# Kernel optimization log

Measured on AMD Instinct MI355X. Metric: run time of the kernel, lower is better.

Reference implementation:

```python
import jax, jax.numpy as jnp
import numpy as np

NUM_HEADS = 16
MASK_VAL = -1e6  # d2l masked_softmax fill value


def setup_inputs() -> dict:
    key = jax.random.key(0)
    ks = jax.random.split(key, 8)
    B, S, D = 4, 1024, 1024
    scale = 1.0 / np.sqrt(D)
    inp = {
        "queries": jax.random.normal(ks[0], (B, S, D), dtype=jnp.float32),
        "keys": jax.random.normal(ks[1], (B, S, D), dtype=jnp.float32),
        "values": jax.random.normal(ks[2], (B, S, D), dtype=jnp.float32),
        "valid_lens": jax.random.randint(ks[3], (B,), 1, S + 1, dtype=jnp.int32),
        "W_q": jax.random.normal(ks[4], (D, D), dtype=jnp.float32) * scale,
        "W_k": jax.random.normal(ks[5], (D, D), dtype=jnp.float32) * scale,
        "W_v": jax.random.normal(ks[6], (D, D), dtype=jnp.float32) * scale,
        "W_o": jax.random.normal(ks[7], (D, D), dtype=jnp.float32) * scale,
    }
    return inp


def _split_heads(x, H):
    # [B, S, D] -> [B, H, S, d]
    B, S, D = x.shape
    return x.reshape(B, S, H, D // H).transpose(0, 2, 1, 3)


def reference(queries, keys, values, valid_lens, W_q, W_k, W_v, W_o):
    H = NUM_HEADS
    B, Sq, D = queries.shape
    Sk = keys.shape[1]
    d = D // H

    q = _split_heads(queries @ W_q.T, H)  # [B, H, Sq, d]
    k = _split_heads(keys @ W_k.T, H)     # [B, H, Sk, d]
    v = _split_heads(values @ W_v.T, H)   # [B, H, Sk, d]

    scores = jnp.einsum("bhqd,bhkd->bhqk", q, k) / jnp.sqrt(jnp.float32(d))
    # masked_softmax: mask key positions >= valid_len (per batch row)
    mask = jnp.arange(Sk)[None, None, None, :] < valid_lens[:, None, None, None]
    scores = jnp.where(mask, scores, MASK_VAL)
    attn = jax.nn.softmax(scores, axis=-1)  # dropout=0.0 -> identity

    out = jnp.einsum("bhqk,bhkd->bhqd", attn, v)  # [B, H, Sq, d]
    out = out.transpose(0, 2, 1, 3).reshape(B, Sq, D)
    return out @ W_o.T
```

## Files before the change

kernel.cpp:

```cpp
#include <hip/hip_runtime.h>

typedef unsigned short ushort_t;
typedef unsigned int uint32;
typedef __attribute__((ext_vector_type(8))) short short8;
typedef __attribute__((ext_vector_type(4))) float float4v;
typedef __attribute__((ext_vector_type(4))) unsigned short ushort4v;

#define NEG_INF (-__builtin_inff())

__device__ __forceinline__ ushort_t f2bf(float f) {
  uint32 u = __float_as_uint(f);
  u += 0x7fffu + ((u >> 16) & 1u);
  return (ushort_t)(u >> 16);
}

__device__ __forceinline__ void glds16(const void* g, void* l) {
  __builtin_amdgcn_global_load_lds(
      (__attribute__((address_space(1))) const void*)g,
      (__attribute__((address_space(3))) void*)l, 16, 0, 0);
}

struct CvtW {
  const float* in[4];
  ushort_t* out[4];
};

__global__ __launch_bounds__(256) void cvt_w_kernel(CvtW a) {
  const float* in = a.in[blockIdx.y];
  ushort_t* out = a.out[blockIdx.y];
  int i = blockIdx.x * 256 + threadIdx.x;
  float4v v = ((const float4v*)in)[i];
  ushort4v o;
  o.x = f2bf(v.x);
  o.y = f2bf(v.y);
  o.z = f2bf(v.z);
  o.w = f2bf(v.w);
  ((ushort4v*)out)[i] = o;
}

struct ProjArgs {
  const float* A[3];
  const ushort_t* B[3];
  ushort_t* C[3];
};

__global__ __launch_bounds__(256) void gemm_proj(ProjArgs pa, int M, int N,
                                                 int K) {
  __shared__ __align__(16) ushort_t Al[128][32];
  __shared__ __align__(16) ushort_t Bl[128][32];
  const int orig = blockIdx.x + (blockIdx.y << 3) + (blockIdx.z << 8);
  const int swz = (orig & 7) * 96 + (orig >> 3);
  const int bn = (swz & 7) * 128;
  const int bm = ((swz >> 3) & 31) * 128;
  const int z = swz >> 8;
  const float* A = pa.A[z];
  const ushort_t* B = pa.B[z];
  ushort_t* C = pa.C[z];
  const int tid = threadIdx.x;
  const int w = tid >> 6, lane = tid & 63;
  const int l15 = lane & 15, lhi = lane >> 4;

  const int wm = (w >> 1) * 64, wn = (w & 1) * 64;

  float4v zero4 = {0.f, 0.f, 0.f, 0.f};
  float4v acc[4][4];
  for (int i = 0; i < 4; i++)
    for (int j = 0; j < 4; j++) acc[i][j] = zero4;

  const int sr = tid >> 2;
  const int sc = tid & 3;
  const int ssw = sc ^ ((sr >> 1) & 3);
  const ushort_t* gb = B + (size_t)(bn + sr) * K + ssw * 8;
  char* lB = (char*)&Bl[0][0];
  const int wb = w * 1024;
  const float* gaf = A + (size_t)(bm + sr) * K + sc * 8;

  const int rsw8 = (lhi ^ ((l15 >> 1) & 3)) * 8;

  for (int kt = 0; kt < K; kt += 32) {
    glds16(gb + kt, lB + wb);
    glds16(gb + (size_t)64 * K + kt, lB + 4096 + wb);
#pragma unroll
    for (int rep = 0; rep < 2; rep++) {
      const int row = rep * 64 + sr;
      const float* p = gaf + (size_t)rep * 64 * K + kt;
      float4v u0 = ((const float4v*)p)[0];
      float4v u1 = ((const float4v*)p)[1];
      short8 sv;
      sv[0] = (short)f2bf(u0.x);
      sv[1] = (short)f2bf(u0.y);
      sv[2] = (short)f2bf(u0.z);
      sv[3] = (short)f2bf(u0.w);
      sv[4] = (short)f2bf(u1.x);
      sv[5] = (short)f2bf(u1.y);
      sv[6] = (short)f2bf(u1.z);
      sv[7] = (short)f2bf(u1.w);
      *(short8*)&Al[row][ssw * 8] = sv;
    }
    __syncthreads();
    short8 af[4], bfr[4];
#pragma unroll
    for (int mi = 0; mi < 4; mi++)
      af[mi] = *(const short8*)&Al[wm + mi * 16 + l15][rsw8];
#pragma unroll
    for (int ni = 0; ni < 4; ni++)
      bfr[ni] = *(const short8*)&Bl[wn + ni * 16 + l15][rsw8];
#pragma unroll
    for (int mi = 0; mi < 4; mi++)
#pragma unroll
      for (int ni = 0; ni < 4; ni++)
        acc[mi][ni] = __builtin_amdgcn_mfma_f32_16x16x32_bf16(
            af[mi], bfr[ni], acc[mi][ni], 0, 0, 0);
    __syncthreads();
  }

#pragma unroll
  for (int mi = 0; mi < 4; mi++)
#pragma unroll
    for (int ni = 0; ni < 4; ni++)
#pragma unroll
      for (int i = 0; i < 4; i++) {
        int row = bm + wm + mi * 16 + lhi * 4 + i;
        int col = bn + wn + ni * 16 + l15;
        C[(size_t)row * N + col] = f2bf(acc[mi][ni][i]);
      }
}

__global__ __launch_bounds__(256) void gemm_out(const ushort_t* __restrict__ A,
                                                const ushort_t* __restrict__ B,
                                                float* __restrict__ Cout, int M,
                                                int N, int K) {
  __shared__ __align__(16) ushort_t Al[128][32];
  __shared__ __align__(16) ushort_t Bl[128][32];
  const int orig = blockIdx.x + (blockIdx.y << 3);
  const int swz = (orig & 7) * 32 + (orig >> 3);
  const int bn = (swz & 7) * 128;
  const int bm = (swz >> 3) * 128;
  const int tid = threadIdx.x;
  const int w = tid >> 6, lane = tid & 63;
  const int l15 = lane & 15, lhi = lane >> 4;
  const int wm = (w >> 1) * 64, wn = (w & 1) * 64;

  float4v zero4 = {0.f, 0.f, 0.f, 0.f};
  float4v acc[4][4];
  for (int i = 0; i < 4; i++)
    for (int j = 0; j < 4; j++) acc[i][j] = zero4;

  const int sr = tid >> 2;
  const int sc = tid & 3;
  const int ssw = sc ^ ((sr >> 1) & 3);
  const ushort_t* ga = A + (size_t)(bm + sr) * K + ssw * 8;
  const ushort_t* gb = B + (size_t)(bn + sr) * K + ssw * 8;
  char* lA = (char*)&Al[0][0];
  char* lB = (char*)&Bl[0][0];
  const int wb = w * 1024;
  const int rsw8 = (lhi ^ ((l15 >> 1) & 3)) * 8;

  for (int kt = 0; kt < K; kt += 32) {
    glds16(ga + kt, lA + wb);
    glds16(ga + (size_t)64 * K + kt, lA + 4096 + wb);
    glds16(gb + kt, lB + wb);
    glds16(gb + (size_t)64 * K + kt, lB + 4096 + wb);
    __syncthreads();
    short8 af[4], bfr[4];
#pragma unroll
    for (int mi = 0; mi < 4; mi++)
      af[mi] = *(const short8*)&Al[wm + mi * 16 + l15][rsw8];
#pragma unroll
    for (int ni = 0; ni < 4; ni++)
      bfr[ni] = *(const short8*)&Bl[wn + ni * 16 + l15][rsw8];
#pragma unroll
    for (int mi = 0; mi < 4; mi++)
#pragma unroll
      for (int ni = 0; ni < 4; ni++)
        acc[mi][ni] = __builtin_amdgcn_mfma_f32_16x16x32_bf16(
            af[mi], bfr[ni], acc[mi][ni], 0, 0, 0);
    __syncthreads();
  }

#pragma unroll
  for (int mi = 0; mi < 4; mi++)
#pragma unroll
    for (int ni = 0; ni < 4; ni++)
#pragma unroll
      for (int i = 0; i < 4; i++) {
        int row = bm + wm + mi * 16 + lhi * 4 + i;
        int col = bn + wn + ni * 16 + l15;
        Cout[(size_t)row * N + col] = acc[mi][ni][i];
      }
}

__global__ __launch_bounds__(256) void transpose_v_kernel(
    const ushort_t* __restrict__ Vp, ushort_t* __restrict__ Vt) {
  __shared__ ushort_t tile[64][65];
  const int bx = blockIdx.x;
  const int b = bx >> 8, h = (bx >> 4) & 15, c = bx & 15;
  const int t = threadIdx.x;
#pragma unroll
  for (int i = 0; i < 16; i++) {
    int id = i * 256 + t;
    int tok = id >> 6, dd = id & 63;
    tile[tok][dd] = Vp[(size_t)(b * 1024 + c * 64 + tok) * 1024 + h * 64 + dd];
  }
  __syncthreads();
#pragma unroll
  for (int i = 0; i < 16; i++) {
    int id = i * 256 + t;
    int dd = id >> 6, tok = id & 63;
    Vt[(size_t)((b * 16 + h) * 64 + dd) * 1024 + c * 64 + tok] = tile[tok][dd];
  }
}

__global__ __launch_bounds__(64) void attn_kernel(
    const ushort_t* __restrict__ Qp, const ushort_t* __restrict__ Kp,
    const ushort_t* __restrict__ Vt, const int* __restrict__ valid_lens,
    ushort_t* __restrict__ Ob) {
  __shared__ __align__(16) ushort_t Plds[16][72];
  const int lane = threadIdx.x & 63;
  const int l15 = lane & 15, lhi = lane >> 4;
  const int bx = blockIdx.x;
  const int b = bx >> 10;
  const int h = (bx >> 6) & 15;
  const int qt = bx & 63;
  const int qrow0 = qt * 16;
  const int vlen = valid_lens[b];

  short8 qf0, qf1;
  {
    const ushort_t* qp =
        Qp + (size_t)(b * 1024 + qrow0 + l15) * 1024 + h * 64 + lhi * 8;
    qf0 = *(const short8*)qp;
    qf1 = *(const short8*)(qp + 32);
  }
  float4v zero4 = {0.f, 0.f, 0.f, 0.f};
  float4v o[4] = {zero4, zero4, zero4, zero4};
  float m_i[4] = {NEG_INF, NEG_INF, NEG_INF, NEG_INF};
  float l_i[4] = {0.f, 0.f, 0.f, 0.f};

  const ushort_t* kh = Kp + (size_t)b * 1024 * 1024 + h * 64;
  const ushort_t* vh = Vt + (size_t)(b * 16 + h) * 64 * 1024;

  for (int kt = 0; kt < 16; kt++) {
    const int k0 = kt * 64;
    if (k0 >= vlen) break;

    float4v s[4];
#pragma unroll
    for (int n = 0; n < 4; n++) {
      const ushort_t* kp = kh + (size_t)(k0 + n * 16 + l15) * 1024 + lhi * 8;
      short8 kf0 = *(const short8*)kp;
      short8 kf1 = *(const short8*)(kp + 32);
      s[n] = __builtin_amdgcn_mfma_f32_16x16x32_bf16(qf0, kf0, zero4, 0, 0, 0);
      s[n] = __builtin_amdgcn_mfma_f32_16x16x32_bf16(qf1, kf1, s[n], 0, 0, 0);
    }
    float pm[4] = {NEG_INF, NEG_INF, NEG_INF, NEG_INF};
#pragma unroll
    for (int n = 0; n < 4; n++) {
      const bool ok = (k0 + n * 16 + l15) < vlen;
#pragma unroll
      for (int i = 0; i < 4; i++) {
        float v = s[n][i] * 0.125f;
        v = ok ? v : -1e6f;
        s[n][i] = v;
        pm[i] = fmaxf(pm[i], v);
      }
    }
#pragma unroll
    for (int d = 1; d < 16; d <<= 1)
#pragma unroll
      for (int i = 0; i < 4; i++) pm[i] = fmaxf(pm[i], __shfl_xor(pm[i], d, 64));

    float alpha[4], rs[4];
#pragma unroll
    for (int i = 0; i < 4; i++) {
      float mn = fmaxf(m_i[i], pm[i]);
      alpha[i] = __expf(m_i[i] - mn);
      m_i[i] = mn;
      rs[i] = 0.f;
    }
#pragma unroll
    for (int n = 0; n < 4; n++)
#pragma unroll
      for (int i = 0; i < 4; i++) {
        float p = __expf(s[n][i] - m_i[i]);
        s[n][i] = p;
        rs[i] += p;
      }
#pragma unroll
    for (int d = 1; d < 16; d <<= 1)
#pragma unroll
      for (int i = 0; i < 4; i++) rs[i] += __shfl_xor(rs[i], d, 64);
#pragma unroll
    for (int i = 0; i < 4; i++) l_i[i] = l_i[i] * alpha[i] + rs[i];
#pragma unroll
    for (int n = 0; n < 4; n++)
#pragma unroll
      for (int i = 0; i < 4; i++) o[n][i] *= alpha[i];

#pragma unroll
    for (int n = 0; n < 4; n++)
#pragma unroll
      for (int i = 0; i < 4; i++)
        Plds[lhi * 4 + i][n * 16 + l15] = f2bf(s[n][i]);

#pragma unroll
    for (int c = 0; c < 2; c++) {
      short8 pa = *(const short8*)&Plds[l15][c * 32 + lhi * 8];
      const ushort_t* vb = vh + k0 + c * 32 + lhi * 8;
#pragma unroll
      for (int n = 0; n < 4; n++) {
        short8 vf = *(const short8*)(vb + (size_t)(n * 16 + l15) * 1024);
        o[n] = __builtin_amdgcn_mfma_f32_16x16x32_bf16(pa, vf, o[n], 0, 0, 0);
      }
    }
  }

#pragma unroll
  for (int n = 0; n < 4; n++)
#pragma unroll
    for (int i = 0; i < 4; i++) {
      float vout = o[n][i] / l_i[i];
      Ob[(size_t)(b * 1024 + qrow0 + lhi * 4 + i) * 1024 + h * 64 + n * 16 +
         l15] = f2bf(vout);
    }
}

extern "C" void kernel_launch(void* const* d_in, const int* in_sizes, int n_in,
                              void* d_out, int out_size, void* d_ws,
                              size_t ws_size, hipStream_t stream) {
  (void)in_sizes;
  (void)n_in;
  (void)out_size;
  (void)ws_size;
  const float* q = (const float*)d_in[0];
  const float* k = (const float*)d_in[1];
  const float* v = (const float*)d_in[2];
  const int* vl = (const int*)d_in[3];
  const float* Wq = (const float*)d_in[4];
  const float* Wk = (const float*)d_in[5];
  const float* Wv = (const float*)d_in[6];
  const float* Wo = (const float*)d_in[7];
  float* out = (float*)d_out;
  char* ws = (char*)d_ws;
  const size_t MB = 1u << 20;

  ushort_t* wqb = (ushort_t*)(ws + 0 * MB);
  ushort_t* wkb = (ushort_t*)(ws + 2 * MB);
  ushort_t* wvb = (ushort_t*)(ws + 4 * MB);
  ushort_t* wob = (ushort_t*)(ws + 6 * MB);
  ushort_t* Qp = (ushort_t*)(ws + 8 * MB);
  ushort_t* Kp = (ushort_t*)(ws + 16 * MB);
  ushort_t* Vp = (ushort_t*)(ws + 24 * MB);
  ushort_t* Vtp = (ushort_t*)(ws + 32 * MB);
  ushort_t* Ob = Vp;

  CvtW cw;
  cw.in[0] = Wq;
  cw.in[1] = Wk;
  cw.in[2] = Wv;
  cw.in[3] = Wo;
  cw.out[0] = wqb;
  cw.out[1] = wkb;
  cw.out[2] = wvb;
  cw.out[3] = wob;
  cvt_w_kernel<<<dim3(1024, 4), 256, 0, stream>>>(cw);

  ProjArgs pa;
  pa.A[0] = q;
  pa.A[1] = k;
  pa.A[2] = v;
  pa.B[0] = wqb;
  pa.B[1] = wkb;
  pa.B[2] = wvb;
  pa.C[0] = Qp;
  pa.C[1] = Kp;
  pa.C[2] = Vp;
  gemm_proj<<<dim3(8, 32, 3), 256, 0, stream>>>(pa, 4096, 1024, 1024);

  transpose_v_kernel<<<1024, 256, 0, stream>>>(Vp, Vtp);
  attn_kernel<<<4096, 64, 0, stream>>>(Qp, Kp, Vtp, vl, Ob);
  gemm_out<<<dim3(8, 32), 256, 0, stream>>>(Ob, wob, out, 4096, 1024, 1024);
}
```

Before: 233.8 us.

## Double-buffer LDS tiles in projection and output GEMMs to overlap loads

Both GEMM kernels now keep two LDS stages and prefetch the next K-tile while MFMAs run on the current one. The projection GEMM holds the fp32 A loads in registers and converts and stores them to LDS after the MFMAs. This halves the number of barriers per K step and hides global load latency, at the cost of double the LDS use and more registers. That may lower occupancy. The global_load_lds writes into the other buffer are issued before the compute, so correctness relies on the barrier at the end of each step.

```diff
diff --git a/kernel.cpp b/kernel.cpp
--- a/kernel.cpp
+++ b/kernel.cpp
@@ -46,8 +46,8 @@
 
 __global__ __launch_bounds__(256) void gemm_proj(ProjArgs pa, int M, int N,
                                                  int K) {
-  __shared__ __align__(16) ushort_t Al[128][32];
-  __shared__ __align__(16) ushort_t Bl[128][32];
+  __shared__ __align__(16) ushort_t Al[2][128][32];
+  __shared__ __align__(16) ushort_t Bl[2][128][32];
   const int orig = blockIdx.x + (blockIdx.y << 3) + (blockIdx.z << 8);
   const int swz = (orig & 7) * 96 + (orig >> 3);
   const int bn = (swz & 7) * 128;
@@ -59,7 +59,6 @@
   const int tid = threadIdx.x;
   const int w = tid >> 6, lane = tid & 63;
   const int l15 = lane & 15, lhi = lane >> 4;
-
   const int wm = (w >> 1) * 64, wn = (w & 1) * 64;
 
   float4v zero4 = {0.f, 0.f, 0.f, 0.f};
@@ -71,47 +70,78 @@
   const int sc = tid & 3;
   const int ssw = sc ^ ((sr >> 1) & 3);
   const ushort_t* gb = B + (size_t)(bn + sr) * K + ssw * 8;
-  char* lB = (char*)&Bl[0][0];
+  char* lBb = (char*)&Bl[0][0][0];
   const int wb = w * 1024;
   const float* gaf = A + (size_t)(bm + sr) * K + sc * 8;
-
   const int rsw8 = (lhi ^ ((l15 >> 1) & 3)) * 8;
-
-  for (int kt = 0; kt < K; kt += 32) {
-    glds16(gb + kt, lB + wb);
-    glds16(gb + (size_t)64 * K + kt, lB + 4096 + wb);
-#pragma unroll
-    for (int rep = 0; rep < 2; rep++) {
-      const int row = rep * 64 + sr;
-      const float* p = gaf + (size_t)rep * 64 * K + kt;
-      float4v u0 = ((const float4v*)p)[0];
-      float4v u1 = ((const float4v*)p)[1];
-      short8 sv;
-      sv[0] = (short)f2bf(u0.x);
-      sv[1] = (short)f2bf(u0.y);
-      sv[2] = (short)f2bf(u0.z);
-      sv[3] = (short)f2bf(u0.w);
-      sv[4] = (short)f2bf(u1.x);
-      sv[5] = (short)f2bf(u1.y);
-      sv[6] = (short)f2bf(u1.z);
-      sv[7] = (short)f2bf(u1.w);
-      *(short8*)&Al[row][ssw * 8] = sv;
-    }
-    __syncthreads();
+  const int NT = K / 32;
+
+  glds16(gb, lBb + wb);
+  glds16(gb + (size_t)64 * K, lBb + 4096 + wb);
+#pragma unroll
+  for (int rep = 0; rep < 2; rep++) {
+    const float* p = gaf + (size_t)rep * 64 * K;
+    float4v u0 = ((const float4v*)p)[0];
+    float4v u1 = ((const float4v*)p)[1];
+    short8 sv;
+    sv[0] = (short)f2bf(u0.x);
+    sv[1] = (short)f2bf(u0.y);
+    sv[2] = (short)f2bf(u0.z);
+    sv[3] = (short)f2bf(u0.w);
+    sv[4] = (short)f2bf(u1.x);
+    sv[5] = (short)f2bf(u1.y);
+    sv[6] = (short)f2bf(u1.z);
+    sv[7] = (short)f2bf(u1.w);
+    *(short8*)&Al[0][rep * 64 + sr][ssw * 8] = sv;
+  }
+  __syncthreads();
+
+  int cur = 0;
+  for (int t = 0; t < NT; ++t) {
+    const int ktn = (t + 1) * 32;
+    const bool pf = (t + 1 < NT);
+    float4v pu0[2], pu1[2];
+    if (pf) {
+      char* lBn = lBb + (cur ^ 1) * 8192;
+      glds16(gb + ktn, lBn + wb);
+      glds16(gb + (size_t)64 * K + ktn, lBn + 4096 + wb);
+#pragma unroll
+      for (int rep = 0; rep < 2; rep++) {
+        const float* p = gaf + (size_t)rep * 64 * K + ktn;
+        pu0[rep] = ((const float4v*)p)[0];
+        pu1[rep] = ((const float4v*)p)[1];
+      }
+    }
     short8 af[4], bfr[4];
 #pragma unroll
     for (int mi = 0; mi < 4; mi++)
-      af[mi] = *(const short8*)&Al[wm + mi * 16 + l15][rsw8];
+      af[mi] = *(const short8*)&Al[cur][wm + mi * 16 + l15][rsw8];
 #pragma unroll
     for (int ni = 0; ni < 4; ni++)
-      bfr[ni] = *(const short8*)&Bl[wn + ni * 16 + l15][rsw8];
+      bfr[ni] = *(const short8*)&Bl[cur][wn + ni * 16 + l15][rsw8];
 #pragma unroll
     for (int mi = 0; mi < 4; mi++)
 #pragma unroll
       for (int ni = 0; ni < 4; ni++)
         acc[mi][ni] = __builtin_amdgcn_mfma_f32_16x16x32_bf16(
             af[mi], bfr[ni], acc[mi][ni], 0, 0, 0);
+    if (pf) {
+#pragma unroll
+      for (int rep = 0; rep < 2; rep++) {
+        short8 sv;
+        sv[0] = (short)f2bf(pu0[rep].x);
+        sv[1] = (short)f2bf(pu0[rep].y);
+        sv[2] = (short)f2bf(pu0[rep].z);
+        sv[3] = (short)f2bf(pu0[rep].w);
+        sv[4] = (short)f2bf(pu1[rep].x);
+        sv[5] = (short)f2bf(pu1[rep].y);
+        sv[6] = (short)f2bf(pu1[rep].z);
+        sv[7] = (short)f2bf(pu1[rep].w);
+        *(short8*)&Al[cur ^ 1][rep * 64 + sr][ssw * 8] = sv;
+      }
+    }
     __syncthreads();
+    cur ^= 1;
   }
 
 #pragma unroll
@@ -130,8 +160,8 @@
                                                 const ushort_t* __restrict__ B,
                                                 float* __restrict__ Cout, int M,
                                                 int N, int K) {
-  __shared__ __align__(16) ushort_t Al[128][32];
-  __shared__ __align__(16) ushort_t Bl[128][32];
+  __shared__ __align__(16) ushort_t Al[2][128][32];
+  __shared__ __align__(16) ushort_t Bl[2][128][32];
   const int orig = blockIdx.x + (blockIdx.y << 3);
   const int swz = (orig & 7) * 32 + (orig >> 3);
   const int bn = (swz & 7) * 128;
@@ -151,24 +181,36 @@
   const int ssw = sc ^ ((sr >> 1) & 3);
   const ushort_t* ga = A + (size_t)(bm + sr) * K + ssw * 8;
   const ushort_t* gb = B + (size_t)(bn + sr) * K + ssw * 8;
-  char* lA = (char*)&Al[0][0];
-  char* lB = (char*)&Bl[0][0];
+  char* lAb = (char*)&Al[0][0][0];
+  char* lBb = (char*)&Bl[0][0][0];
   const int wb = w * 1024;
   const int rsw8 = (lhi ^ ((l15 >> 1) & 3)) * 8;
-
-  for (int kt = 0; kt < K; kt += 32) {
-    glds16(ga + kt, lA + wb);
-    glds16(ga + (size_t)64 * K + kt, lA + 4096 + wb);
-    glds16(gb + kt, lB + wb);
-    glds16(gb + (size_t)64 * K + kt, lB + 4096 + wb);
-    __syncthreads();
+  const int NT = K / 32;
+
+  glds16(ga, lAb + wb);
+  glds16(ga + (size_t)64 * K, lAb + 4096 + wb);
+  glds16(gb, lBb + wb);
+  glds16(gb + (size_t)64 * K, lBb + 4096 + wb);
+  __syncthreads();
+
+  int cur = 0;
+  for (int t = 0; t < NT; ++t) {
+    const int ktn = (t + 1) * 32;
+    if (t + 1 < NT) {
+      char* lAn = lAb + (cur ^ 1) * 8192;
+      char* lBn = lBb + (cur ^ 1) * 8192;
+      glds16(ga + ktn, lAn + wb);
+      glds16(ga + (size_t)64 * K + ktn, lAn + 4096 + wb);
+      glds16(gb + ktn, lBn + wb);
+      glds16(gb + (size_t)64 * K + ktn, lBn + 4096 + wb);
+    }
     short8 af[4], bfr[4];
 #pragma unroll
     for (int mi = 0; mi < 4; mi++)
-      af[mi] = *(const short8*)&Al[wm + mi * 16 + l15][rsw8];
+      af[mi] = *(const short8*)&Al[cur][wm + mi * 16 + l15][rsw8];
 #pragma unroll
     for (int ni = 0; ni < 4; ni++)
-      bfr[ni] = *(const short8*)&Bl[wn + ni * 16 + l15][rsw8];
+      bfr[ni] = *(const short8*)&Bl[cur][wn + ni * 16 + l15][rsw8];
 #pragma unroll
     for (int mi = 0; mi < 4; mi++)
 #pragma unroll
@@ -176,6 +218,7 @@
         acc[mi][ni] = __builtin_amdgcn_mfma_f32_16x16x32_bf16(
             af[mi], bfr[ni], acc[mi][ni], 0, 0, 0);
     __syncthreads();
+    cur ^= 1;
   }
 
 #pragma unroll
```

After: 225.0 us. 3.7% less time.
